# Kernel tuning notes

Hardware: AMD Instinct MI355X
Metric: run time of the kernel (lower is better)

The kernel has to match this reference:

```python
import jax, jax.numpy as jnp
import numpy as np

H, W, P = 480, 600, 2048
N = H * W
_IU = np.triu_indices(4)

def _conv(x, w, b, stride=1):
    y = jax.lax.conv_general_dilated(x, w, (stride, stride), 'SAME',
                                     dimension_numbers=('NCHW', 'OIHW', 'NCHW'))
    return y + b[None, :, None, None]

def _gn(x, scale, bias, groups=16, eps=1e-5):
    n, c, h, w = x.shape
    xg = x.reshape(n, groups, c // groups, h, w)
    mu = xg.mean(axis=(2, 3, 4), keepdims=True)
    var = xg.var(axis=(2, 3, 4), keepdims=True)
    xg = (xg - mu) * jax.lax.rsqrt(var + eps)
    return xg.reshape(n, c, h, w) * scale[None, :, None, None] + bias[None, :, None, None]

def _lrelu(x):
    return jnp.where(x >= 0, x, 0.2 * x)

def setup_inputs():
    key = jax.random.key(0)
    ks = jax.random.split(key, 16)
    def he(k, shape, fan_in):
        return jax.random.normal(k, shape, jnp.float32) * np.float32(np.sqrt(2.0 / fan_in))
    return {
        'depth': jax.random.normal(ks[0], (1, 1, H, W), jnp.float32),
        'pose': jax.random.normal(ks[1], (P, 2, 8), jnp.float32),
        'target_mask': (jax.random.uniform(ks[2], (1, 1, H, W)) > 0.5).astype(jnp.float32),
        'pairs': jax.random.randint(ks[3], (P, 2), 0, N),
        'conv1_w': he(ks[4], (32, 3, 3, 3), 3 * 9), 'conv1_b': jnp.zeros(32),
        'gn1_s': jnp.ones(32), 'gn1_b': jnp.zeros(32),
        'conv2_w': he(ks[5], (64, 32, 3, 3), 32 * 9), 'conv2_b': jnp.zeros(64),
        'gn2_s': jnp.ones(64), 'gn2_b': jnp.zeros(64),
        'conv3_w': he(ks[6], (64, 64, 3, 3), 64 * 9), 'conv3_b': jnp.zeros(64),
        'gn3_s': jnp.ones(64), 'gn3_b': jnp.zeros(64),
        'conv4_w': he(ks[7], (64, 96, 3, 3), 96 * 9), 'conv4_b': jnp.zeros(64),
        'gn4_s': jnp.ones(64), 'gn4_b': jnp.zeros(64),
        'gate_w': he(ks[8], (15, 64), 15), 'gate_b': jnp.zeros(64),
        'hid_w': he(ks[9], (64, 64), 64), 'hid_b': jnp.zeros(64),
        'out_w': he(ks[10], (64, 1), 64), 'out_b': jnp.zeros(1),
    }

def _forward(depth, pose, target_mask, params, pairs):
    (c1w, c1b, g1s, g1b, c2w, c2b, g2s, g2b, c3w, c3b, g3s, g3b,
     c4w, c4b, g4s, g4b, gw, gb, hw_, hb, ow, ob) = params
    idx = pairs[:, 0]
    hh, ww = idx // W, idx % W
    # vectorized replacement of the per-pair python-loop scatter
    attn = jnp.zeros((1, 1, H, W), jnp.float32).at[0, 0, hh, ww].set(1.0)
    std_depth = (depth - depth.mean()) * 10.0
    x = jnp.concatenate([std_depth, target_mask, attn], axis=1)  # [1,3,H,W]
    # res_unet backbone (encoder-decoder, GroupNorm, leaky-relu 0.2)
    c1 = _lrelu(_gn(_conv(x, c1w, c1b), g1s, g1b))               # [1,32,H,W]
    d1 = _lrelu(_gn(_conv(c1, c2w, c2b, stride=2), g2s, g2b))    # [1,64,H/2,W/2]
    bm = _lrelu(_gn(_conv(d1, c3w, c3b), g3s, g3b))              # [1,64,H/2,W/2]
    up = jax.image.resize(bm, (1, 64, H, W), method='nearest')
    u = jnp.concatenate([up, c1], axis=1)                         # [1,96,H,W]
    feats = _lrelu(_gn(_conv(u, c4w, c4b), g4s, g4b))            # [1,64,H,W]
    # vectorized per-pair gather
    fg = feats.reshape(64, N)[:, idx].T                           # [P,64]
    fg = jnp.broadcast_to(fg[:, None, :], (P, 2, 64))
    dg = std_depth.reshape(N)[idx]
    dg = jnp.broadcast_to(dg[:, None, None], (P, 2, 1))
    quat = pose[:, :, :4]
    fingers = pose[:, :, 4:7]
    trans = pose[:, :, 7:8]
    outer = quat[..., :, None] * quat[..., None, :]               # sign-invariant q_i*q_j
    enc = outer[..., _IU[0], _IU[1]]                              # [P,2,10]
    cond = jnp.concatenate([enc, fingers, trans, dg], axis=-1)    # [P,2,15]
    # ContextGate_1d: gated attention over gathered features
    gate = jax.nn.sigmoid(cond @ gw + gb)                         # [P,2,64]
    h = fg * gate
    h = h * jax.lax.rsqrt(jnp.sum(h * h, axis=-1, keepdims=True) + 1e-8)
    h = _lrelu(h @ hw_ + hb)
    return jax.nn.silu(h) @ ow + ob                               # [P,2,1]

def reference(depth, pose, target_mask, pairs, conv1_w, conv1_b, gn1_s, gn1_b,
              conv2_w, conv2_b, gn2_s, gn2_b, conv3_w, conv3_b, gn3_s, gn3_b,
              conv4_w, conv4_b, gn4_s, gn4_b, gate_w, gate_b, hid_w, hid_b,
              out_w, out_b):
    params = (conv1_w, conv1_b, gn1_s, gn1_b, conv2_w, conv2_b, gn2_s, gn2_b,
              conv3_w, conv3_b, gn3_s, gn3_b, conv4_w, conv4_b, gn4_s, gn4_b,
              gate_w, gate_b, hid_w, hid_b, out_w, out_b)
    return _forward(depth, pose, target_mask, params, pairs)
```

## Files before the change

### kernel.cpp

```cpp
#include <hip/hip_runtime.h>
#include <math.h>

#define HH 480
#define WW 600
#define NN (HH*WW)
#define PP 2048
#define H2 240
#define W2 300
#define N2 (H2*W2)

typedef __bf16  bf16x8  __attribute__((ext_vector_type(8)));
typedef __bf16  bf16x4  __attribute__((ext_vector_type(4)));
typedef float   f32x4   __attribute__((ext_vector_type(4)));
typedef ushort  ushort8 __attribute__((ext_vector_type(8)));

__device__ __forceinline__ ushort f2b(float f) {
    unsigned u = __float_as_uint(f);
    unsigned r = (u + 0x7FFF + ((u >> 16) & 1)) >> 16;
    return (ushort)r;
}

constexpr size_t alup(size_t x) { return (x + 4095) & ~(size_t)4095; }
constexpr size_t OFF_X    = 4096;
constexpr size_t OFF_C1R  = alup(OFF_X   + 3UL*NN*4);
constexpr size_t OFF_RW2  = alup(OFF_C1R + 32UL*NN*2);
constexpr size_t OFF_RW3  = alup(OFF_RW2 + 64UL*N2*2);
constexpr size_t OFF_WB2  = alup(OFF_RW3 + 64UL*N2*2);
constexpr size_t OFF_WB3  = alup(OFF_WB2 + 36864UL);
constexpr size_t OFF_WB4  = alup(OFF_WB3 + 73728UL);
constexpr size_t OFF_SLOT = alup(OFF_WB4 + 110592UL);
constexpr size_t OFF_CMP  = alup(OFF_SLOT + (size_t)NN*4);

__global__ void k_sum(const float* __restrict__ d, float* __restrict__ ws) {
    float s = 0.f;
    for (int i = blockIdx.x*blockDim.x + threadIdx.x; i < NN; i += gridDim.x*blockDim.x)
        s += d[i];
    #pragma unroll
    for (int o = 32; o; o >>= 1) s += __shfl_down(s, o, 64);
    __shared__ float sm[4];
    int wid = threadIdx.x >> 6;
    if ((threadIdx.x & 63) == 0) sm[wid] = s;
    __syncthreads();
    if (threadIdx.x == 0) {
        float t = 0.f;
        for (int w = 0; w < (int)(blockDim.x >> 6); ++w) t += sm[w];
        atomicAdd(ws, t);
    }
}

__global__ void k_buildx(const float* __restrict__ depth, const float* __restrict__ mask,
                         const float* __restrict__ ws, float* __restrict__ x) {
    int i = blockIdx.x*blockDim.x + threadIdx.x;
    if (i >= NN) return;
    float mean = ws[0] * (1.0f/NN);
    x[i]        = (depth[i] - mean) * 10.0f;
    x[NN + i]   = mask[i];
    x[2*NN + i] = 0.f;
}

__global__ void k_scatter(const int* __restrict__ pairs, float* __restrict__ x) {
    int p = blockIdx.x*blockDim.x + threadIdx.x;
    if (p < PP) x[2*NN + pairs[2*p]] = 1.0f;
}

__global__ void k_slot(const int* __restrict__ pairs, int* __restrict__ slotmap) {
    int p = blockIdx.x*blockDim.x + threadIdx.x;
    if (p < PP) slotmap[pairs[2*p]] = p;
}

__global__ void k_wcvt(const float* __restrict__ w, ushort* __restrict__ dst, int NCH) {
    int e = blockIdx.x*256 + threadIdx.x;
    int total = 9*NCH*64*32;
    if (e >= total) return;
    int k  = e & 31;
    int co = (e >> 5) & 63;
    int rest = e >> 11;
    int c = rest % NCH;
    int t = rest / NCH;
    dst[e] = f2b(w[(co*(NCH*32) + c*32 + k)*9 + t]);
}

template<int CIN, int TCO, int YPB>
__global__ __launch_bounds__(64) void k_conv1(const float* __restrict__ in,
        const float* __restrict__ w, const float* __restrict__ bias,
        ushort* __restrict__ outb, float* __restrict__ stat) {
    int x    = blockIdx.x*64 + threadIdx.x;
    int lane = threadIdx.x;
    int co0  = blockIdx.z*TCO;
    bool valid = x < WW;
    float s[TCO/2], s2[TCO/2];
    #pragma unroll
    for (int j = 0; j < TCO/2; ++j) { s[j] = 0.f; s2[j] = 0.f; }

    int  xb   = x - 1;
    bool xint = (xb >= 0) && (xb + 2 < WW);

    for (int yy = 0; yy < YPB; ++yy) {
        int y = blockIdx.y*YPB + yy;
        float acc[TCO];
        #pragma unroll
        for (int c = 0; c < TCO; ++c) acc[c] = bias[co0+c];
        for (int ci = 0; ci < CIN; ++ci) {
            const float* ip = in + (long)ci*NN;
            float iv[3][3];
            #pragma unroll
            for (int dy = 0; dy < 3; ++dy) {
                int iy = y + dy - 1;
                if ((unsigned)iy < (unsigned)HH) {
                    const float* rp = ip + (long)iy*WW + xb;
                    if (xint) { iv[dy][0]=rp[0]; iv[dy][1]=rp[1]; iv[dy][2]=rp[2]; }
                    else {
                        #pragma unroll
                        for (int dx = 0; dx < 3; ++dx) {
                            int ix = xb + dx;
                            iv[dy][dx] = ((unsigned)ix < (unsigned)WW) ? ip[(long)iy*WW+ix] : 0.f;
                        }
                    }
                } else iv[dy][0]=iv[dy][1]=iv[dy][2]=0.f;
            }
            const float* wp = w + ((long)co0*CIN + ci)*9;
            #pragma unroll
            for (int c = 0; c < TCO; ++c)
                #pragma unroll
                for (int k = 0; k < 9; ++k)
                    acc[c] += iv[k/3][k%3] * wp[(long)c*CIN*9 + k];
        }
        if (valid) {
            bf16x8 p0, p1;
            #pragma unroll
            for (int j = 0; j < 8; ++j) { p0[j] = (__bf16)acc[j]; p1[j] = (__bf16)acc[8+j]; }
            ushort* op = outb + (size_t)(y*WW + x)*32 + co0;
            *(ushort8*)op     = __builtin_bit_cast(ushort8, p0);
            *(ushort8*)(op+8) = __builtin_bit_cast(ushort8, p1);
            #pragma unroll
            for (int j = 0; j < TCO/2; ++j) {
                float a = acc[2*j], b = acc[2*j+1];
                s[j]  += a + b;
                s2[j] += a*a + b*b;
            }
        }
    }

    #pragma unroll
    for (int o = 1; o < 64; o <<= 1)
        #pragma unroll
        for (int j = 0; j < TCO/2; ++j) {
            s[j]  += __shfl_xor(s[j],  o, 64);
            s2[j] += __shfl_xor(s2[j], o, 64);
        }
    float vs = 0.f, vq = 0.f;
    #pragma unroll
    for (int j = 0; j < TCO/2; ++j) {
        vs = (lane == j)         ? s[j]  : vs;
        vq = (lane == j + TCO/2) ? s2[j] : vq;
    }
    if (lane < TCO) {
        int g0 = co0 >> 1;
        int addr = (lane < TCO/2) ? (g0 + lane) : (16 + g0 + lane - TCO/2);
        atomicAdd(&stat[addr], (lane < TCO/2) ? vs : vq);
    }
}

template<int MODE>
__global__ __launch_bounds__(256) void k_sconv(
        const ushort* __restrict__ inA, const ushort* __restrict__ inB,
        const ushort* __restrict__ wb, const float* __restrict__ bias,
        const float* __restrict__ gsA, const float* __restrict__ gbA, const float* __restrict__ stA,
        const float* __restrict__ gsB, const float* __restrict__ gbB, const float* __restrict__ stB,
        ushort* __restrict__ outb,
        const int* __restrict__ slotmap, float* __restrict__ compact,
        float* __restrict__ stat) {
    constexpr int Wo   = (MODE==4) ? WW : W2;
    constexpr int NCH  = (MODE==2) ? 1 : (MODE==3) ? 2 : 3;
    constexpr int NPT  = (MODE==2) ? 2 : 4;
    constexpr int ROWS = (MODE==2) ? 9 : 6;
    constexpr int PXS  = 68;
    constexpr int CPITCH = 36;
    constexpr int UNITS = ROWS*PXS*4;
    constexpr int NLD  = (UNITS + 255)/256;
    constexpr int Hi = (MODE==3) ? H2 : HH;
    constexpr int Wi = (MODE==3) ? W2 : WW;
    __shared__ __align__(16) ushort sh[ROWS*PXS*CPITCH];
    __shared__ float sred[4][16][2];

    int w    = threadIdx.x >> 6;
    int lane = threadIdx.x & 63;
    int lm   = lane & 15;
    int lg   = lane >> 4;
    int q    = threadIdx.x & 3;
    int y0   = blockIdx.y*4;
    int x0   = blockIdx.x*(NPT*16);
    int y    = y0 + w;
    int iy0  = (MODE==2) ? 2*y0 : y0 - 1;
    int ix0  = (MODE==2) ? 2*x0 : x0 - 1;

    f32x4 acc[4][NPT];
    #pragma unroll
    for (int ct = 0; ct < 4; ++ct)
        #pragma unroll
        for (int pt = 0; pt < NPT; ++pt) acc[ct][pt] = 0.f;

    int dsbase = (((MODE==2 ? 2*w*PXS + 2*lm : w*PXS + lm))*CPITCH + lg*8);

    ushort8  stg[NLD];
    unsigned vmask = 0;

    auto LOADR = [&](int kc) {
        vmask = 0;
        #pragma unroll
        for (int i = 0; i < NLD; ++i) {
            int u = i*256 + (int)threadIdx.x;
            ushort8 v = {};
            if (u < UNITS) {
                int r  = u / (PXS*4);
                int rm = u - r*(PXS*4);
                int px = rm >> 2;
                int iy = iy0 + r;
                int ix = ix0 + px;
                if ((unsigned)iy < (unsigned)Hi && (unsigned)ix < (unsigned)Wi) {
                    const ushort* sp;
                    if (MODE==2)      sp = inA + ((size_t)iy*WW + ix)*32 + q*8;
                    else if (MODE==3) sp = inA + ((size_t)iy*W2 + ix)*64 + kc*32 + q*8;
                    else if (kc < 2)  sp = inA + ((size_t)(iy>>1)*W2 + (ix>>1))*64 + kc*32 + q*8;
                    else              sp = inB + ((size_t)iy*WW + ix)*32 + q*8;
                    v = *(const ushort8*)sp;
                    vmask |= (1u << i);
                }
            }
            stg[i] = v;
        }
    };

    LOADR(0);

    #pragma unroll
    for (int kc = 0; kc < NCH; ++kc) {
        float Ac[8], Bc[8];
        {
            const bool useB = (MODE==4) && (kc == 2);
            const float* gs = useB ? gsB : gsA;
            const float* gb = useB ? gbB : gbA;
            const float* st = useB ? stB : stA;
            const float cnt = (MODE==2 || useB) ? 2.0f*(float)NN : 4.0f*(float)N2;
            const int   shp = (MODE==2 || useB) ? 1 : 2;
            const int   cb  = (MODE==2 || useB) ? q*8 : kc*32 + q*8;
            #pragma unroll
            for (int j = 0; j < 8; ++j) {
                int c = cb + j, g = c >> shp;
                float mu  = st[g] / cnt;
                float var = st[16+g] / cnt - mu*mu;
                float rs  = rsqrtf(var + 1e-5f);
                float a   = rs * gs[c];
                Ac[j] = a; Bc[j] = gb[c] - mu*a;
            }
        }
        if (kc) __syncthreads();
        #pragma unroll
        for (int i = 0; i < NLD; ++i) {
            int u = i*256 + (int)threadIdx.x;
            if (u < UNITS) {
                int r  = u / (PXS*4);
                int rm = u - r*(PXS*4);
                int px = rm >> 2;
                bf16x8 raw = __builtin_bit_cast(bf16x8, stg[i]);
                bool val = (vmask >> i) & 1;
                bf16x8 o;
                #pragma unroll
                for (int j = 0; j < 8; ++j) {
                    float t = (float)raw[j]*Ac[j] + Bc[j];
                    t = fmaxf(t, 0.2f*t);
                    o[j] = (__bf16)(val ? t : 0.f);
                }
                *(ushort8*)&sh[(r*PXS + px)*CPITCH + q*8] = __builtin_bit_cast(ushort8, o);
            }
        }
        __syncthreads();
        if (kc + 1 < NCH) LOADR(kc + 1);
        #pragma unroll
        for (int t = 0; t < 9; ++t) {
            const int dy = t/3, dx = t - 3*(t/3);
            const ushort* wp = wb + (size_t)((t*NCH + kc)*64)*32;
            bf16x8 a[4];
            #pragma unroll
            for (int ct = 0; ct < 4; ++ct)
                a[ct] = *(const bf16x8*)(wp + (ct*16 + lm)*32 + lg*8);
            #pragma unroll
            for (int pt = 0; pt < NPT; ++pt) {
                int off = (dy*PXS + (MODE==2 ? pt*32 + dx : pt*16 + dx))*CPITCH;
                bf16x8 b = *(const bf16x8*)&sh[dsbase + off];
                #pragma unroll
                for (int ct = 0; ct < 4; ++ct)
                    acc[ct][pt] = __builtin_amdgcn_mfma_f32_16x16x32_bf16(a[ct], b, acc[ct][pt], 0, 0, 0);
            }
        }
    }

    if (MODE != 4) {
        #pragma unroll
        for (int ct = 0; ct < 4; ++ct) {
            float s = 0.f, s2 = 0.f;
            #pragma unroll
            for (int pt = 0; pt < NPT; ++pt) {
                int pxg = x0 + pt*16 + lm;
                bool vld = pxg < Wo;
                bf16x4 pk;
                #pragma unroll
                for (int reg = 0; reg < 4; ++reg) {
                    int co = ct*16 + lg*4 + reg;
                    float v = acc[ct][pt][reg] + bias[co];
                    pk[reg] = (__bf16)v;
                    if (vld) { s += v; s2 += v*v; }
                }
                if (vld)
                    *(bf16x4*)(outb + (size_t)(y*Wo + pxg)*64 + ct*16 + lg*4) = pk;
            }
            #pragma unroll
            for (int o = 1; o < 16; o <<= 1) {
                s  += __shfl_xor(s,  o, 64);
                s2 += __shfl_xor(s2, o, 64);
            }
            if (lm == 0) { sred[w][ct*4+lg][0] = s; sred[w][ct*4+lg][1] = s2; }
        }
    } else {
        int slots[4];
        #pragma unroll
        for (int pt = 0; pt < 4; ++pt) {
            int pxg = x0 + pt*16 + lm;
            slots[pt] = (pxg < Wo) ? slotmap[(size_t)y*Wo + pxg] : -1;
        }
        #pragma unroll
        for (int ct = 0; ct < 4; ++ct) {
            float s = 0.f, s2 = 0.f;
            #pragma unroll
            for (int pt = 0; pt < 4; ++pt) {
                int pxg = x0 + pt*16 + lm;
                bool vld = pxg < Wo;
                f32x4 r;
                #pragma unroll
                for (int reg = 0; reg < 4; ++reg) {
                    int co = ct*16 + lg*4 + reg;
                    float v = acc[ct][pt][reg] + bias[co];
                    r[reg] = v;
                    if (vld) { s += v; s2 += v*v; }
                }
                if (slots[pt] >= 0)
                    *(f32x4*)(compact + (size_t)slots[pt]*64 + ct*16 + lg*4) = r;
            }
            #pragma unroll
            for (int o = 1; o < 16; o <<= 1) {
                s  += __shfl_xor(s,  o, 64);
                s2 += __shfl_xor(s2, o, 64);
            }
            if (lm == 0) { sred[w][ct*4+lg][0] = s; sred[w][ct*4+lg][1] = s2; }
        }
    }
    __syncthreads();
    if (threadIdx.x < 32) {
        int g = threadIdx.x >> 1, k = threadIdx.x & 1;
        float t = sred[0][g][k] + sred[1][g][k] + sred[2][g][k] + sred[3][g][k];
        atomicAdd(&stat[k*16 + g], t);
    }
}

__global__ void k_mlp(const float* __restrict__ pose, const float* __restrict__ sd,
                      const int* __restrict__ pairs, const int* __restrict__ slotmap,
                      const float* __restrict__ compact,
                      const float* __restrict__ g4s, const float* __restrict__ g4b,
                      const float* __restrict__ st4,
                      const float* __restrict__ gw, const float* __restrict__ gb,
                      const float* __restrict__ hw, const float* __restrict__ hb,
                      const float* __restrict__ ow, const float* __restrict__ ob,
                      float* __restrict__ out) {
    int wid  = threadIdx.x >> 6;
    int lane = threadIdx.x & 63;
    int t = blockIdx.x*4 + wid;
    int p = t >> 1;
    const float* pp = pose + t*8;
    float q0=pp[0], q1=pp[1], q2=pp[2], q3=pp[3];
    float f0=pp[4], f1=pp[5], f2=pp[6], tr=pp[7];
    int idx = pairs[2*p];
    float dg = sd[idx];
    float cond[15] = {q0*q0,q0*q1,q0*q2,q0*q3,q1*q1,q1*q2,q1*q3,q2*q2,q2*q3,q3*q3,
                      f0,f1,f2,tr,dg};
    float acc = gb[lane];
    #pragma unroll
    for (int k = 0; k < 15; ++k) acc += cond[k]*gw[k*64+lane];
    float gate = 1.f/(1.f+expf(-acc));
    int slot = slotmap[idx];
    float raw = compact[(size_t)slot*64 + lane];
    int   g4  = lane >> 2;
    float cnt = 4.0f * (float)NN;
    float mu  = st4[g4] / cnt;
    float var = st4[16+g4] / cnt - mu*mu;
    float rs  = rsqrtf(var + 1e-5f);
    float fv  = (raw - mu) * rs * g4s[lane] + g4b[lane];
    float fg  = fv >= 0.f ? fv : 0.2f*fv;
    float h = fg*gate;
    float ss = h*h;
    #pragma unroll
    for (int o = 32; o; o >>= 1) ss += __shfl_xor(ss, o, 64);
    h *= rsqrtf(ss + 1e-8f);
    __shared__ float hs[4][64];
    hs[wid][lane] = h;
    __syncthreads();
    float a2 = hb[lane];
    #pragma unroll 8
    for (int d = 0; d < 64; ++d) a2 += hs[wid][d]*hw[d*64+lane];
    float h2 = a2 >= 0.f ? a2 : 0.2f*a2;
    float si = h2 / (1.f+expf(-h2));
    float v = si * ow[lane];
    #pragma unroll
    for (int o = 32; o; o >>= 1) v += __shfl_xor(v, o, 64);
    if (lane == 0) out[t] = v + ob[0];
}

extern "C" void kernel_launch(void* const* d_in, const int* in_sizes, int n_in,
                              void* d_out, int out_size, void* d_ws, size_t ws_size,
                              hipStream_t stream) {
    const float* depth = (const float*)d_in[0];
    const float* pose  = (const float*)d_in[1];
    const float* mask  = (const float*)d_in[2];
    const int*   pairs = (const int*)  d_in[3];
    const float* c1w = (const float*)d_in[4];  const float* c1b = (const float*)d_in[5];
    const float* g1s = (const float*)d_in[6];  const float* g1b = (const float*)d_in[7];
    const float* c2w = (const float*)d_in[8];  const float* c2b = (const float*)d_in[9];
    const float* g2s = (const float*)d_in[10]; const float* g2b = (const float*)d_in[11];
    const float* c3w = (const float*)d_in[12]; const float* c3b = (const float*)d_in[13];
    const float* g3s = (const float*)d_in[14]; const float* g3b = (const float*)d_in[15];
    const float* c4w = (const float*)d_in[16]; const float* c4b = (const float*)d_in[17];
    const float* g4s = (const float*)d_in[18]; const float* g4b = (const float*)d_in[19];
    const float* gw  = (const float*)d_in[20]; const float* gb  = (const float*)d_in[21];
    const float* hw_ = (const float*)d_in[22]; const float* hb  = (const float*)d_in[23];
    const float* ow  = (const float*)d_in[24]; const float* ob  = (const float*)d_in[25];

    char* base = (char*)d_ws;
    float*  stats = (float*) base;
    float*  X    = (float*) (base + OFF_X);
    ushort* C1R  = (ushort*)(base + OFF_C1R);
    ushort* RW2  = (ushort*)(base + OFF_RW2);
    ushort* RW3  = (ushort*)(base + OFF_RW3);
    ushort* WB2  = (ushort*)(base + OFF_WB2);
    ushort* WB3  = (ushort*)(base + OFF_WB3);
    ushort* WB4  = (ushort*)(base + OFF_WB4);
    int*    SLOT = (int*)   (base + OFF_SLOT);
    float*  CMP  = (float*) (base + OFF_CMP);
    float* st1 = stats + 16;
    float* st2 = stats + 64;
    float* st3 = stats + 112;
    float* st4 = stats + 160;

    hipMemsetAsync(d_ws, 0, 1024, stream);
    hipMemsetAsync(SLOT, 0xFF, (size_t)NN*4, stream);

    k_sum    <<<1024, 256, 0, stream>>>(depth, stats);
    k_buildx <<<(NN+255)/256, 256, 0, stream>>>(depth, mask, stats, X);
    k_scatter<<<(PP+255)/256, 256, 0, stream>>>(pairs, X);
    k_slot   <<<(PP+255)/256, 256, 0, stream>>>(pairs, SLOT);
    k_wcvt   <<< 72, 256, 0, stream>>>(c2w, WB2, 1);
    k_wcvt   <<<144, 256, 0, stream>>>(c3w, WB3, 2);
    k_wcvt   <<<216, 256, 0, stream>>>(c4w, WB4, 3);

    k_conv1<3,16,8><<<dim3(10, 60, 2), 64, 0, stream>>>(X, c1w, c1b, C1R, st1);

    k_sconv<2><<<dim3(10, 60), 256, 0, stream>>>(C1R, nullptr, WB2, c2b,
        g1s, g1b, st1, nullptr, nullptr, nullptr, RW2, nullptr, nullptr, st2);

    k_sconv<3><<<dim3(5, 60), 256, 0, stream>>>(RW2, nullptr, WB3, c3b,
        g2s, g2b, st2, nullptr, nullptr, nullptr, RW3, nullptr, nullptr, st3);

    k_sconv<4><<<dim3(10, 120), 256, 0, stream>>>(RW3, C1R, WB4, c4b,
        g3s, g3b, st3, g1s, g1b, st1, nullptr, SLOT, CMP, st4);

    k_mlp<<<(2*PP)/4, 256, 0, stream>>>(pose, X, pairs, SLOT, CMP, g4s, g4b, st4,
                                        gw, gb, hw_, hb, ow, ob, (float*)d_out);
}
```

Baseline: 317.0 us.

## Pre-normalize activations into zero-padded buffers and stage conv tiles via direct global-to-LDS loads

GroupNorm and leaky-ReLU are no longer applied inside each conv's tile loader. Separate k_gnpack passes now write normalized bf16 activations into zero-bordered padded buffers, and k_borders zeroes the pads. The conv kernels then copy tiles straight into LDS with global_load_lds using an XOR swizzle, which removes bounds checks, register staging and per-element math. The cost is extra kernel launches and an extra read and write of each activation tensor, plus changed grid shapes for conv1 and conv3 and the loss of the register prefetch of the next channel chunk.

```diff
diff --git a/kernel.cpp b/kernel.cpp
--- a/kernel.cpp
+++ b/kernel.cpp
@@ -19,13 +19,25 @@
     unsigned r = (u + 0x7FFF + ((u >> 16) & 1)) >> 16;
     return (ushort)r;
 }
-
-constexpr size_t alup(size_t x) { return (x + 4095) & ~(size_t)4095; }
-constexpr size_t OFF_X    = 4096;
-constexpr size_t OFF_C1R  = alup(OFF_X   + 3UL*NN*4);
-constexpr size_t OFF_RW2  = alup(OFF_C1R + 32UL*NN*2);
-constexpr size_t OFF_RW3  = alup(OFF_RW2 + 64UL*N2*2);
-constexpr size_t OFF_WB2  = alup(OFF_RW3 + 64UL*N2*2);
+__device__ __forceinline__ float b2f(ushort u) {
+    return __uint_as_float(((unsigned)u) << 16);
+}
+
+__device__ __forceinline__ void gl_lds16(const ushort* g, ushort* l) {
+    __builtin_amdgcn_global_load_lds(
+        (const __attribute__((address_space(1))) unsigned int*)g,
+        (__attribute__((address_space(3))) unsigned int*)l, 16, 0, 0);
+}
+
+constexpr size_t alup(size_t x) { return (x + 65535) & ~(size_t)65535; }
+constexpr size_t OFF_X    = 65536;
+constexpr size_t OFF_C1R  = alup(OFF_X    + 3UL*NN*4);
+constexpr size_t OFF_C1N  = alup(OFF_C1R  + 32UL*NN*2);
+constexpr size_t OFF_RW2R = alup(OFF_C1N  + 482UL*602*32*2 + 65536);
+constexpr size_t OFF_RW2N = alup(OFF_RW2R + 64UL*N2*2);
+constexpr size_t OFF_RW3R = alup(OFF_RW2N + 242UL*302*64*2 + 65536);
+constexpr size_t OFF_RW3N = alup(OFF_RW3R + 64UL*N2*2);
+constexpr size_t OFF_WB2  = alup(OFF_RW3N + 242UL*302*64*2 + 65536);
 constexpr size_t OFF_WB3  = alup(OFF_WB2 + 36864UL);
 constexpr size_t OFF_WB4  = alup(OFF_WB3 + 73728UL);
 constexpr size_t OFF_SLOT = alup(OFF_WB4 + 110592UL);
@@ -66,6 +78,23 @@
 __global__ void k_slot(const int* __restrict__ pairs, int* __restrict__ slotmap) {
     int p = blockIdx.x*blockDim.x + threadIdx.x;
     if (p < PP) slotmap[pairs[2*p]] = p;
+}
+
+__global__ void k_borders(ushort* __restrict__ c1n, ushort* __restrict__ rw2n,
+                          ushort* __restrict__ rw3n) {
+    int i = blockIdx.x*256 + threadIdx.x;
+    ushort* buf; int Hp, Wp, upp, j = i;
+    if (i < 8656)            { buf = c1n;  Hp = 482; Wp = 602; upp = 4; }
+    else if (i < 17328)      { buf = rw2n; Hp = 242; Wp = 302; upp = 8; j = i - 8656; }
+    else if (i < 26000)      { buf = rw3n; Hp = 242; Wp = 302; upp = 8; j = i - 17328; }
+    else return;
+    int px = j / upp, oct = j - (j/upp)*upp;
+    int y, x;
+    if (px < Wp)        { y = 0;      x = px; }
+    else if (px < 2*Wp) { y = Hp - 1; x = px - Wp; }
+    else { int s = px - 2*Wp; y = 1 + (s >> 1); x = (s & 1) ? Wp - 1 : 0; }
+    ushort8 z = {};
+    *(ushort8*)&buf[((size_t)y*Wp + x)*(upp*8) + oct*8] = z;
 }
 
 __global__ void k_wcvt(const float* __restrict__ w, ushort* __restrict__ dst, int NCH) {
@@ -161,33 +190,53 @@
     }
 }
 
+template<int C, int CHPER>
+__global__ __launch_bounds__(256) void k_gnpack(const ushort* __restrict__ raw,
+        ushort* __restrict__ outp, const float* __restrict__ gs,
+        const float* __restrict__ gb, const float* __restrict__ st,
+        int Wwd, float cnt) {
+    constexpr int UPP = C/8;
+    int y = blockIdx.y;
+    int e = blockIdx.x*256 + threadIdx.x;
+    if (e >= Wwd*UPP) return;
+    int x   = e / UPP;
+    int oct = e - x*UPP;
+    int c0  = oct*8;
+    ushort8 r = *(const ushort8*)&raw[((size_t)y*Wwd + x)*C + c0];
+    bf16x8 o;
+    #pragma unroll
+    for (int j = 0; j < 8; ++j) {
+        int c = c0 + j, g = c / CHPER;
+        float mu  = st[g] / cnt;
+        float var = st[16+g] / cnt - mu*mu;
+        float rs  = rsqrtf(var + 1e-5f);
+        float v = (b2f(r[j]) - mu) * rs * gs[c] + gb[c];
+        o[j] = (__bf16)fmaxf(v, 0.2f*v);
+    }
+    *(ushort8*)&outp[(((size_t)y + 1)*(Wwd + 2) + x + 1)*C + c0] = __builtin_bit_cast(ushort8, o);
+}
+
 template<int MODE>
 __global__ __launch_bounds__(256) void k_sconv(
         const ushort* __restrict__ inA, const ushort* __restrict__ inB,
         const ushort* __restrict__ wb, const float* __restrict__ bias,
-        const float* __restrict__ gsA, const float* __restrict__ gbA, const float* __restrict__ stA,
-        const float* __restrict__ gsB, const float* __restrict__ gbB, const float* __restrict__ stB,
         ushort* __restrict__ outb,
         const int* __restrict__ slotmap, float* __restrict__ compact,
         float* __restrict__ stat) {
     constexpr int Wo   = (MODE==4) ? WW : W2;
     constexpr int NCH  = (MODE==2) ? 1 : (MODE==3) ? 2 : 3;
-    constexpr int NPT  = (MODE==2) ? 2 : 4;
+    constexpr int NPT  = (MODE==4) ? 4 : 2;
     constexpr int ROWS = (MODE==2) ? 9 : 6;
-    constexpr int PXS  = 68;
-    constexpr int CPITCH = 36;
+    constexpr int PXS  = (MODE==3) ? 36 : 68;
     constexpr int UNITS = ROWS*PXS*4;
     constexpr int NLD  = (UNITS + 255)/256;
-    constexpr int Hi = (MODE==3) ? H2 : HH;
-    constexpr int Wi = (MODE==3) ? W2 : WW;
-    __shared__ __align__(16) ushort sh[ROWS*PXS*CPITCH];
+    __shared__ __align__(16) ushort sh[UNITS*8];
     __shared__ float sred[4][16][2];
 
     int w    = threadIdx.x >> 6;
     int lane = threadIdx.x & 63;
     int lm   = lane & 15;
     int lg   = lane >> 4;
-    int q    = threadIdx.x & 3;
     int y0   = blockIdx.y*4;
     int x0   = blockIdx.x*(NPT*16);
     int y    = y0 + w;
@@ -200,60 +249,8 @@
         #pragma unroll
         for (int pt = 0; pt < NPT; ++pt) acc[ct][pt] = 0.f;
 
-    int dsbase = (((MODE==2 ? 2*w*PXS + 2*lm : w*PXS + lm))*CPITCH + lg*8);
-
-    ushort8  stg[NLD];
-    unsigned vmask = 0;
-
-    auto LOADR = [&](int kc) {
-        vmask = 0;
-        #pragma unroll
-        for (int i = 0; i < NLD; ++i) {
-            int u = i*256 + (int)threadIdx.x;
-            ushort8 v = {};
-            if (u < UNITS) {
-                int r  = u / (PXS*4);
-                int rm = u - r*(PXS*4);
-                int px = rm >> 2;
-                int iy = iy0 + r;
-                int ix = ix0 + px;
-                if ((unsigned)iy < (unsigned)Hi && (unsigned)ix < (unsigned)Wi) {
-                    const ushort* sp;
-                    if (MODE==2)      sp = inA + ((size_t)iy*WW + ix)*32 + q*8;
-                    else if (MODE==3) sp = inA + ((size_t)iy*W2 + ix)*64 + kc*32 + q*8;
-                    else if (kc < 2)  sp = inA + ((size_t)(iy>>1)*W2 + (ix>>1))*64 + kc*32 + q*8;
-                    else              sp = inB + ((size_t)iy*WW + ix)*32 + q*8;
-                    v = *(const ushort8*)sp;
-                    vmask |= (1u << i);
-                }
-            }
-            stg[i] = v;
-        }
-    };
-
-    LOADR(0);
-
     #pragma unroll
     for (int kc = 0; kc < NCH; ++kc) {
-        float Ac[8], Bc[8];
-        {
-            const bool useB = (MODE==4) && (kc == 2);
-            const float* gs = useB ? gsB : gsA;
-            const float* gb = useB ? gbB : gbA;
-            const float* st = useB ? stB : stA;
-            const float cnt = (MODE==2 || useB) ? 2.0f*(float)NN : 4.0f*(float)N2;
-            const int   shp = (MODE==2 || useB) ? 1 : 2;
-            const int   cb  = (MODE==2 || useB) ? q*8 : kc*32 + q*8;
-            #pragma unroll
-            for (int j = 0; j < 8; ++j) {
-                int c = cb + j, g = c >> shp;
-                float mu  = st[g] / cnt;
-                float var = st[16+g] / cnt - mu*mu;
-                float rs  = rsqrtf(var + 1e-5f);
-                float a   = rs * gs[c];
-                Ac[j] = a; Bc[j] = gb[c] - mu*a;
-            }
-        }
         if (kc) __syncthreads();
         #pragma unroll
         for (int i = 0; i < NLD; ++i) {
@@ -262,20 +259,20 @@
                 int r  = u / (PXS*4);
                 int rm = u - r*(PXS*4);
                 int px = rm >> 2;
-                bf16x8 raw = __builtin_bit_cast(bf16x8, stg[i]);
-                bool val = (vmask >> i) & 1;
-                bf16x8 o;
-                #pragma unroll
-                for (int j = 0; j < 8; ++j) {
-                    float t = (float)raw[j]*Ac[j] + Bc[j];
-                    t = fmaxf(t, 0.2f*t);
-                    o[j] = (__bf16)(val ? t : 0.f);
-                }
-                *(ushort8*)&sh[(r*PXS + px)*CPITCH + q*8] = __builtin_bit_cast(ushort8, o);
+                int qp = rm & 3;
+                int q  = (MODE==2) ? (qp ^ ((px>>1)&3) ^ ((px>>3)&3))
+                                   : (qp ^ (px&3) ^ ((px>>2)&3));
+                int iy = iy0 + r;
+                int ix = ix0 + px;
+                const ushort* sp;
+                if (MODE==2)      sp = inA + ((size_t)(iy+1)*602 + (ix+1))*32 + q*8;
+                else if (MODE==3) sp = inA + ((size_t)(iy+1)*302 + (ix+1))*64 + kc*32 + q*8;
+                else if (kc < 2)  sp = inA + ((size_t)((iy>>1)+1)*302 + ((ix>>1)+1))*64 + kc*32 + q*8;
+                else              sp = inB + ((size_t)(iy+1)*602 + (ix+1))*32 + q*8;
+                gl_lds16(sp, &sh[(size_t)u*8]);
             }
         }
         __syncthreads();
-        if (kc + 1 < NCH) LOADR(kc + 1);
         #pragma unroll
         for (int t = 0; t < 9; ++t) {
             const int dy = t/3, dx = t - 3*(t/3);
@@ -284,10 +281,14 @@
             #pragma unroll
             for (int ct = 0; ct < 4; ++ct)
                 a[ct] = *(const bf16x8*)(wp + (ct*16 + lm)*32 + lg*8);
+            int rr = (MODE==2) ? (2*w + dy) : (w + dy);
             #pragma unroll
             for (int pt = 0; pt < NPT; ++pt) {
-                int off = (dy*PXS + (MODE==2 ? pt*32 + dx : pt*16 + dx))*CPITCH;
-                bf16x8 b = *(const bf16x8*)&sh[dsbase + off];
+                int pxl = (MODE==2) ? (2*lm + pt*32 + dx) : (pt*16 + lm + dx);
+                int swz = (MODE==2) ? (((pxl>>1)&3) ^ ((pxl>>3)&3))
+                                    : ((pxl&3) ^ ((pxl>>2)&3));
+                int unit = (rr*PXS + pxl)*4 + (lg ^ swz);
+                bf16x8 b = *(const bf16x8*)&sh[(size_t)unit*8];
                 #pragma unroll
                 for (int ct = 0; ct < 4; ++ct)
                     acc[ct][pt] = __builtin_amdgcn_mfma_f32_16x16x32_bf16(a[ct], b, acc[ct][pt], 0, 0, 0);
@@ -437,8 +438,11 @@
     float*  stats = (float*) base;
     float*  X    = (float*) (base + OFF_X);
     ushort* C1R  = (ushort*)(base + OFF_C1R);
-    ushort* RW2  = (ushort*)(base + OFF_RW2);
-    ushort* RW3  = (ushort*)(base + OFF_RW3);
+    ushort* C1N  = (ushort*)(base + OFF_C1N);
+    ushort* RW2R = (ushort*)(base + OFF_RW2R);
+    ushort* RW2N = (ushort*)(base + OFF_RW2N);
+    ushort* RW3R = (ushort*)(base + OFF_RW3R);
+    ushort* RW3N = (ushort*)(base + OFF_RW3N);
     ushort* WB2  = (ushort*)(base + OFF_WB2);
     ushort* WB3  = (ushort*)(base + OFF_WB3);
     ushort* WB4  = (ushort*)(base + OFF_WB4);
@@ -456,20 +460,24 @@
     k_buildx <<<(NN+255)/256, 256, 0, stream>>>(depth, mask, stats, X);
     k_scatter<<<(PP+255)/256, 256, 0, stream>>>(pairs, X);
     k_slot   <<<(PP+255)/256, 256, 0, stream>>>(pairs, SLOT);
+    k_borders<<<102, 256, 0, stream>>>(C1N, RW2N, RW3N);
     k_wcvt   <<< 72, 256, 0, stream>>>(c2w, WB2, 1);
     k_wcvt   <<<144, 256, 0, stream>>>(c3w, WB3, 2);
     k_wcvt   <<<216, 256, 0, stream>>>(c4w, WB4, 3);
 
-    k_conv1<3,16,8><<<dim3(10, 60, 2), 64, 0, stream>>>(X, c1w, c1b, C1R, st1);
-
-    k_sconv<2><<<dim3(10, 60), 256, 0, stream>>>(C1R, nullptr, WB2, c2b,
-        g1s, g1b, st1, nullptr, nullptr, nullptr, RW2, nullptr, nullptr, st2);
-
-    k_sconv<3><<<dim3(5, 60), 256, 0, stream>>>(RW2, nullptr, WB3, c3b,
-        g2s, g2b, st2, nullptr, nullptr, nullptr, RW3, nullptr, nullptr, st3);
-
-    k_sconv<4><<<dim3(10, 120), 256, 0, stream>>>(RW3, C1R, WB4, c4b,
-        g3s, g3b, st3, g1s, g1b, st1, nullptr, SLOT, CMP, st4);
+    k_conv1<3,16,2><<<dim3(10, 240, 2), 64, 0, stream>>>(X, c1w, c1b, C1R, st1);
+    k_gnpack<32,2><<<dim3(10, 480), 256, 0, stream>>>(C1R, C1N, g1s, g1b, st1, WW, 2.0f*NN);
+
+    k_sconv<2><<<dim3(10, 60), 256, 0, stream>>>(C1N, nullptr, WB2, c2b,
+        RW2R, nullptr, nullptr, st2);
+    k_gnpack<64,4><<<dim3(10, 240), 256, 0, stream>>>(RW2R, RW2N, g2s, g2b, st2, W2, 4.0f*N2);
+
+    k_sconv<3><<<dim3(10, 60), 256, 0, stream>>>(RW2N, nullptr, WB3, c3b,
+        RW3R, nullptr, nullptr, st3);
+    k_gnpack<64,4><<<dim3(10, 240), 256, 0, stream>>>(RW3R, RW3N, g3s, g3b, st3, W2, 4.0f*N2);
+
+    k_sconv<4><<<dim3(10, 120), 256, 0, stream>>>(RW3N, C1N, WB4, c4b,
+        nullptr, SLOT, CMP, st4);
 
     k_mlp<<<(2*PP)/4, 256, 0, stream>>>(pose, X, pairs, SLOT, CMP, g4s, g4b, st4,
                                         gw, gb, hw_, hb, ow, ob, (float*)d_out);
```

Result: slower. 352.1 us (+11.1%).
